# Kernel tuning notes

Measured on AMD Instinct MI355X. Metric: run time of the kernel, lower is better.

## Reference

```python
import jax, jax.numpy as jnp
import numpy as np
from jax.scipy.special import gammainc, gammaln

M, N, D, L, J = 64, 2048, 256, 64, 384  # queries, train points, feat dim, buckets, ncx2 series terms
SIGMA2 = 4.0          # sigma=2.0
BUCKET_SHRINK = 1.0
NEG = -999999.0


def _make_buckets():
    # Mirrors fit(): linspace(ncx2.ppf(1e-4, D*shrink, 0), ncx2.ppf(1-1e-4, D, D*shrink/sigma2)) * sigma2,
    # using the normal approximation to the (non)central chi-square quantiles (scipy unavailable).
    z = 3.7190165  # Phi^{-1}(0.9999)
    df = float(D)
    nc0 = df * BUCKET_SHRINK / SIGMA2
    lb = df * BUCKET_SHRINK - z * np.sqrt(2.0 * df * BUCKET_SHRINK)
    ub = (df + nc0) + z * np.sqrt(2.0 * (df + 2.0 * nc0))
    return jnp.asarray(np.linspace(lb, ub, L) * SIGMA2, dtype=jnp.float32)


def setup_inputs() -> dict:
    key = jax.random.key(0)
    k1, k2, k3 = jax.random.split(key, 3)
    X = jax.random.normal(k1, (M, D), dtype=jnp.float32)
    train_X = jax.random.normal(k2, (N, D), dtype=jnp.float32)
    train_y = jax.random.randint(k3, (N,), 0, 2, dtype=jnp.int32)
    buckets = _make_buckets()
    return {"X": X, "train_X": train_X, "buckets": buckets, "train_y": train_y}


def _ncx2_cdf_matrix(nc, buckets):
    # ncx2.cdf(x, df=D, nc) = sum_j Pois(nc/2)[j] * gammainc(D/2 + j, x/2)
    # nc: [M, N]; buckets are the (already /sigma2) CDF evaluation points x: [L]
    half_nc = nc * 0.5                                            # [M, N]
    j = jnp.arange(J, dtype=jnp.float32)                          # [J]
    logw = (-half_nc[..., None] + j * jnp.log(half_nc)[..., None]
            - gammaln(j + 1.0))                                   # [M, N, J]
    w = jnp.exp(logw)
    G = gammainc(0.5 * D + j[:, None], 0.5 * buckets[None, :])    # [J, L]
    return jnp.einsum('mnj,jl->mnl', w, G)                        # [M, N, L]


def _predict(X, train_X, buckets, train_y):
    # squared euclidean distances, [M, N]
    dists = (jnp.sum(X * X, -1)[:, None] + jnp.sum(train_X * train_X, -1)[None, :]
             - 2.0 * (X @ train_X.T))
    dists = jnp.maximum(dists, 0.0)
    F = _ncx2_cdf_matrix(dists / SIGMA2, buckets / SIGMA2)        # [M, N, L]
    p_mat = jnp.concatenate([F[..., 1:] - F[..., :-1], 1.0 - F[..., -1:]], axis=-1)  # [M, N, L]
    psum = jnp.cumsum(p_mat[..., ::-1], axis=-1)[..., ::-1]       # reverse cumsum over buckets
    logpprod = jnp.cumsum(jnp.log(jnp.maximum(psum, 1e-30)), axis=1)  # scan over train points
    logpprod = jnp.maximum(logpprod, NEG)
    logpprod = jnp.where(jnp.isnan(logpprod), NEG, logpprod)
    # term1[i, l] = logpprod[i-1, l+1] (0 for i==0; NEG at l==L-1 for i>0)
    inner = logpprod[:, :-1, 1:]                                  # [M, N-1, L-1]
    term1 = jnp.concatenate([inner, jnp.full((M, N - 1, 1), NEG, dtype=inner.dtype)], axis=-1)
    term1 = jnp.concatenate([jnp.zeros((M, 1, L), dtype=inner.dtype), term1], axis=1)  # [M, N, L]
    term2 = logpprod[:, -1:, :] - logpprod                        # [M, N, L]
    p = jnp.sum(p_mat * jnp.exp(term1 + term2), axis=-1)          # [M, N] per-point KNN prob
    onehot = jax.nn.one_hot(train_y, 2, dtype=p.dtype)            # [N, 2]
    pred = p @ onehot                                             # [M, 2]
    return pred / jnp.sum(pred, axis=-1, keepdims=True)


def reference(X, train_X, buckets, train_y):
    return _predict(X, train_X, buckets, train_y)
```

## Files before the change

kernel.cpp:

```cpp
#include <hip/hip_runtime.h>
#include <math.h>

#define M_ 64
#define N_ 2048
#define D_ 256
#define L_ 64
#define J_ 384
#define CHUNKS 32
#define CN 64

typedef _Float16 half8 __attribute__((ext_vector_type(8)));
typedef float f32x4 __attribute__((ext_vector_type(4)));

#define OFF_F16   0u
#define OFF_LG8   49152u
#define OFF_INV   49344u
#define OFF_SQX   50880u
#define OFF_PRED  51136u
#define OFF_CHUNK 576000u
#define OFF_PSUM  1657344u

__global__ __launch_bounds__(64)
void k_tab(const float* __restrict__ buckets, const float* __restrict__ Xg,
           char* __restrict__ ws) {
    _Float16* F16 = (_Float16*)(ws + OFF_F16);
    float* lg8  = (float*)(ws + OFF_LG8);
    float* invt = (float*)(ws + OFF_INV);
    float* sqX  = (float*)(ws + OFF_SQX);
    float* pred = (float*)(ws + OFF_PRED);
    int jg = blockIdx.x, l = threadIdx.x;

    if (jg < 12) {
        double x = (double)buckets[l] * 0.125;
        double a = 128.0 + 32.0 * (double)jg;
        double gln = lgamma(a);
        double q;
        if (x < a + 1.0) {
            double ap = a, sum = 1.0 / a, del = sum;
            for (int it = 0; it < 3000; ++it) {
                ap += 1.0; del *= x / ap; sum += del;
                if (fabs(del) < fabs(sum) * 1e-16) break;
            }
            q = 1.0 - sum * exp(-x + a * log(x) - gln);
        } else {
            double b = x + 1.0 - a, c = 1e300, d = 1.0 / b, h = d;
            for (int i = 1; i <= 3000; ++i) {
                double an = -(double)i * ((double)i - a);
                b += 2.0;
                d = an * d + b; if (fabs(d) < 1e-300) d = 1e-300;
                c = b + an / c; if (fabs(c) < 1e-300) c = 1e-300;
                d = 1.0 / d;
                double delc = d * c; h *= delc;
                if (fabs(delc - 1.0) < 1e-16) break;
            }
            q = exp(-x + a * log(x) - gln) * h;
        }
        double tt = exp(a * log(x) - x - lgamma(a + 1.0));
        for (int jj = 0; jj < 32; ++jj) {
            double F = 1.0 - q;
            if (F < 0.0) F = 0.0;
            F16[l * J_ + (jg << 5) + jj] = (_Float16)F;
            q += tt; if (q > 1.0) q = 1.0;
            tt *= x / (a + (double)jj + 1.0);
        }
    } else {
        const float4* xr = (const float4*)(Xg + l * D_);
        float s0 = 0, s1 = 0, s2 = 0, s3 = 0;
        for (int k = 0; k < D_ / 4; ++k) {
            float4 v = xr[k];
            s0 = fmaf(v.x, v.x, s0); s1 = fmaf(v.y, v.y, s1);
            s2 = fmaf(v.z, v.z, s2); s3 = fmaf(v.w, v.w, s3);
        }
        sqX[l] = (s0 + s1) + (s2 + s3);
        if (l < 48) lg8[l] = (float)lgamma(8.0 * (double)l + 1.0);
        for (int i = l; i < J_; i += 64) invt[i] = 1.0f / (float)(i + 1);
        pred[2 * l] = 0.f; pred[2 * l + 1] = 0.f;
    }
}

__global__ __launch_bounds__(128)
void k_fused(const float* __restrict__ Xg, const float* __restrict__ TXg,
             char* __restrict__ ws) {
    const _Float16* F16 = (const _Float16*)(ws + OFF_F16);
    const float* lg8    = (const float*)(ws + OFF_LG8);
    const float* invt   = (const float*)(ws + OFF_INV);
    const float* sqX    = (const float*)(ws + OFF_SQX);
    float* psum         = (float*)(ws + OFF_PSUM);
    double* chunk       = (double*)(ws + OFF_CHUNK);

    __shared__ float  s_dist[64];
    __shared__ double s_part[2][64];

    int bid = blockIdx.x;
    int m = bid >> 5, c = bid & 31;
    int n0 = c << 6;
    int t = threadIdx.x;

    {
        int nloc = t >> 1, half = t & 1;
        const float4* T4 = (const float4*)(TXg + (size_t)(n0 + nloc) * D_ + (half << 7));
        const float4* X4 = (const float4*)(Xg + m * D_ + (half << 7));
        float4 dd{0,0,0,0}, ss{0,0,0,0};
#pragma unroll 8
        for (int k = 0; k < 32; ++k) {
            float4 tv = T4[k], xv = X4[k];
            dd.x = fmaf(xv.x, tv.x, dd.x); dd.y = fmaf(xv.y, tv.y, dd.y);
            dd.z = fmaf(xv.z, tv.z, dd.z); dd.w = fmaf(xv.w, tv.w, dd.w);
            ss.x = fmaf(tv.x, tv.x, ss.x); ss.y = fmaf(tv.y, tv.y, ss.y);
            ss.z = fmaf(tv.z, tv.z, ss.z); ss.w = fmaf(tv.w, tv.w, ss.w);
        }
        float dot = (dd.x + dd.y) + (dd.z + dd.w);
        float st  = (ss.x + ss.y) + (ss.z + ss.w);
        dot += __shfl_xor(dot, 1);
        st  += __shfl_xor(st, 1);
        if (half == 0)
            s_dist[nloc] = fmaxf(sqX[m] + st - 2.f * dot, 0.f);
    }
    __syncthreads();

    int w = t >> 6, l = t & 63;
    int col = l & 15, g = l >> 4;
    int rbase = n0 + (w << 5);

    float la0 = s_dist[(w << 5) + col]      * 0.125f;
    float la1 = s_dist[(w << 5) + 16 + col] * 0.125f;
    float ll0 = __logf(la0), ll1 = __logf(la1);

    f32x4 acc00 = {0,0,0,0}, acc01 = {0,0,0,0}, acc02 = {0,0,0,0}, acc03 = {0,0,0,0};
    f32x4 acc10 = {0,0,0,0}, acc11 = {0,0,0,0}, acc12 = {0,0,0,0}, acc13 = {0,0,0,0};

    for (int s = 0; s < 12; ++s) {
        int jb = (s << 5) + (g << 3);
        float jbf = (float)jb;
        half8 b0 = *(const half8*)(F16 + (size_t)(col     ) * J_ + jb);
        half8 b1 = *(const half8*)(F16 + (size_t)(col + 16) * J_ + jb);
        half8 b2 = *(const half8*)(F16 + (size_t)(col + 32) * J_ + jb);
        half8 b3 = *(const half8*)(F16 + (size_t)(col + 48) * J_ + jb);
        float lgv = lg8[(s << 2) + g];
        float4 iv0 = *(const float4*)(invt + jb);
        float4 iv1 = *(const float4*)(invt + jb + 4);
        {
            float wv = __expf(fmaf(jbf, ll0, -la0 - lgv));
            half8 a;
            a[0] = (_Float16)wv;
            wv *= la0 * iv0.x; a[1] = (_Float16)wv;
            wv *= la0 * iv0.y; a[2] = (_Float16)wv;
            wv *= la0 * iv0.z; a[3] = (_Float16)wv;
            wv *= la0 * iv0.w; a[4] = (_Float16)wv;
            wv *= la0 * iv1.x; a[5] = (_Float16)wv;
            wv *= la0 * iv1.y; a[6] = (_Float16)wv;
            wv *= la0 * iv1.z; a[7] = (_Float16)wv;
            acc00 = __builtin_amdgcn_mfma_f32_16x16x32_f16(a, b0, acc00, 0, 0, 0);
            acc01 = __builtin_amdgcn_mfma_f32_16x16x32_f16(a, b1, acc01, 0, 0, 0);
            acc02 = __builtin_amdgcn_mfma_f32_16x16x32_f16(a, b2, acc02, 0, 0, 0);
            acc03 = __builtin_amdgcn_mfma_f32_16x16x32_f16(a, b3, acc03, 0, 0, 0);
        }
        {
            float wv = __expf(fmaf(jbf, ll1, -la1 - lgv));
            half8 a;
            a[0] = (_Float16)wv;
            wv *= la1 * iv0.x; a[1] = (_Float16)wv;
            wv *= la1 * iv0.y; a[2] = (_Float16)wv;
            wv *= la1 * iv0.z; a[3] = (_Float16)wv;
            wv *= la1 * iv0.w; a[4] = (_Float16)wv;
            wv *= la1 * iv1.x; a[5] = (_Float16)wv;
            wv *= la1 * iv1.y; a[6] = (_Float16)wv;
            wv *= la1 * iv1.z; a[7] = (_Float16)wv;
            acc10 = __builtin_amdgcn_mfma_f32_16x16x32_f16(a, b0, acc10, 0, 0, 0);
            acc11 = __builtin_amdgcn_mfma_f32_16x16x32_f16(a, b1, acc11, 0, 0, 0);
            acc12 = __builtin_amdgcn_mfma_f32_16x16x32_f16(a, b2, acc12, 0, 0, 0);
            acc13 = __builtin_amdgcn_mfma_f32_16x16x32_f16(a, b3, acc13, 0, 0, 0);
        }
    }

    double lsum0 = 0.0, lsum1 = 0.0, lsum2 = 0.0, lsum3 = 0.0;
    float* pbase = psum + (((size_t)(m << 11) + rbase) << 6);
#define EPI(ACC, SP, TI, LS)                                                    \
    {                                                                           \
        _Pragma("unroll")                                                       \
        for (int r = 0; r < 4; ++r) {                                           \
            float ps = 1.f - (ACC)[r];                                          \
            int row = (SP) * 16 + g * 4 + r;                                    \
            pbase[((size_t)row << 6) + (TI) * 16 + col] = ps;                   \
            LS += (double)__logf(fmaxf(ps, 1e-30f));                            \
        }                                                                       \
    }
    EPI(acc00, 0, 0, lsum0) EPI(acc01, 0, 1, lsum1) EPI(acc02, 0, 2, lsum2) EPI(acc03, 0, 3, lsum3)
    EPI(acc10, 1, 0, lsum0) EPI(acc11, 1, 1, lsum1) EPI(acc12, 1, 2, lsum2) EPI(acc13, 1, 3, lsum3)
#undef EPI
    lsum0 += __shfl_xor(lsum0, 16); lsum0 += __shfl_xor(lsum0, 32);
    lsum1 += __shfl_xor(lsum1, 16); lsum1 += __shfl_xor(lsum1, 32);
    lsum2 += __shfl_xor(lsum2, 16); lsum2 += __shfl_xor(lsum2, 32);
    lsum3 += __shfl_xor(lsum3, 16); lsum3 += __shfl_xor(lsum3, 32);
    if (g == 0) {
        s_part[w][col]      = lsum0;
        s_part[w][16 + col] = lsum1;
        s_part[w][32 + col] = lsum2;
        s_part[w][48 + col] = lsum3;
    }
    __syncthreads();
    if (t < 64)
        chunk[((m << 5) + c) * 64 + t] = s_part[0][t] + s_part[1][t];
}

__global__ __launch_bounds__(64)
void k_scan(const int* __restrict__ ty, char* __restrict__ ws) {
    const float* psum   = (const float*)(ws + OFF_PSUM);
    const double* chunk = (const double*)(ws + OFF_CHUNK);
    float* pred         = (float*)(ws + OFF_PRED);
    int b = blockIdx.x, m = b >> 5, c = b & (CHUNKS - 1), l = threadIdx.x;

    double cum = 0.0, T = 0.0;
    for (int c2 = 0; c2 < CHUNKS; ++c2) {
        double v = chunk[((m << 5) + c2) * 64 + l];
        T += v;
        if (c2 < c) cum += v;
    }

    const float* P = psum + (((size_t)m * N_ + (size_t)c * CN) << 6);
    int n0 = c * CN;
    float a0 = 0.f, a1 = 0.f;
    for (int i = 0; i < CN; ++i) {
        float pv = P[((size_t)i << 6) + l];
        float lv = __logf(fmaxf(pv, 1e-30f));
        double nbr = __shfl_down(cum, 1);
        float pvn  = __shfl_down(pv, 1);
        double cin = cum + (double)lv;
        int n = n0 + i;
        double t1 = (n == 0) ? 0.0 : ((l == 63) ? -999999.0 : nbr);
        double t2 = T - cin;
        float e = (float)(t1 + t2);
        float pm = (l == 63) ? pv : (pv - pvn);
        float contrib = pm * __expf(e);
        int y = ty[n];
        a0 += (y == 0) ? contrib : 0.f;
        a1 += (y == 1) ? contrib : 0.f;
        cum = cin;
    }
#pragma unroll
    for (int o = 32; o > 0; o >>= 1) {
        a0 += __shfl_down(a0, o);
        a1 += __shfl_down(a1, o);
    }
    if (l == 0) {
        atomicAdd(&pred[m * 2 + 0], a0);
        atomicAdd(&pred[m * 2 + 1], a1);
    }
}

__global__ __launch_bounds__(64)
void k_norm(char* __restrict__ ws, float* __restrict__ out) {
    const float* pred = (const float*)(ws + OFF_PRED);
    int m = threadIdx.x;
    float a = pred[2 * m], b = pred[2 * m + 1];
    float s = a + b;
    out[2 * m]     = a / s;
    out[2 * m + 1] = b / s;
}

extern "C" void kernel_launch(void* const* d_in, const int* in_sizes, int n_in,
                              void* d_out, int out_size, void* d_ws, size_t ws_size,
                              hipStream_t stream) {
    const float* X       = (const float*)d_in[0];
    const float* train_X = (const float*)d_in[1];
    const float* buckets = (const float*)d_in[2];
    const int*   train_y = (const int*)d_in[3];
    float* out = (float*)d_out;
    char*  ws  = (char*)d_ws;

    k_tab<<<13, 64, 0, stream>>>(buckets, X, ws);
    k_fused<<<M_ * CHUNKS, 128, 0, stream>>>(X, train_X, ws);
    k_scan<<<M_ * CHUNKS, 64, 0, stream>>>(train_y, ws);
    k_norm<<<1, 64, 0, stream>>>(ws, out);
}
```

Measured before the change: 168.1 us.

## Skip negligible Poisson-weight slabs, parallelize gamma table, finer scan chunks

```diff
diff --git a/kernel.cpp b/kernel.cpp
--- a/kernel.cpp
+++ b/kernel.cpp
@@ -4,21 +4,20 @@
 #define M_ 64
 #define N_ 2048
 #define D_ 256
-#define L_ 64
 #define J_ 384
-#define CHUNKS 32
-#define CN 64
+#define C2N 64
+#define CN2 32
 
 typedef _Float16 half8 __attribute__((ext_vector_type(8)));
 typedef float f32x4 __attribute__((ext_vector_type(4)));
 
 #define OFF_F16   0u
 #define OFF_LG8   49152u
-#define OFF_INV   49344u
-#define OFF_SQX   50880u
-#define OFF_PRED  51136u
-#define OFF_CHUNK 576000u
-#define OFF_PSUM  1657344u
+#define OFF_INV   49408u
+#define OFF_SQX   50944u
+#define OFF_PRED  51200u
+#define OFF_CHUNK 51712u
+#define OFF_PSUM  2148864u
 
 __global__ __launch_bounds__(64)
 void k_tab(const float* __restrict__ buckets, const float* __restrict__ Xg,
@@ -30,36 +29,35 @@
     float* pred = (float*)(ws + OFF_PRED);
     int jg = blockIdx.x, l = threadIdx.x;
 
-    if (jg < 12) {
-        double x = (double)buckets[l] * 0.125;
-        double a = 128.0 + 32.0 * (double)jg;
+    if (jg < 48) {
+        const double x = (double)buckets[l] * 0.125;
+        const double a = 128.0 + 8.0 * (double)jg;
         double gln = lgamma(a);
         double q;
         if (x < a + 1.0) {
             double ap = a, sum = 1.0 / a, del = sum;
-            for (int it = 0; it < 3000; ++it) {
+            for (int it = 0; it < 2000; ++it) {
                 ap += 1.0; del *= x / ap; sum += del;
                 if (fabs(del) < fabs(sum) * 1e-16) break;
             }
             q = 1.0 - sum * exp(-x + a * log(x) - gln);
         } else {
-            double b = x + 1.0 - a, c = 1e300, d = 1.0 / b, h = d;
-            for (int i = 1; i <= 3000; ++i) {
+            double b = x + 1.0 - a, cc = 1e300, d = 1.0 / b, h = d;
+            for (int i = 1; i <= 2000; ++i) {
                 double an = -(double)i * ((double)i - a);
                 b += 2.0;
                 d = an * d + b; if (fabs(d) < 1e-300) d = 1e-300;
-                c = b + an / c; if (fabs(c) < 1e-300) c = 1e-300;
+                cc = b + an / cc; if (fabs(cc) < 1e-300) cc = 1e-300;
                 d = 1.0 / d;
-                double delc = d * c; h *= delc;
+                double delc = d * cc; h *= delc;
                 if (fabs(delc - 1.0) < 1e-16) break;
             }
             q = exp(-x + a * log(x) - gln) * h;
         }
         double tt = exp(a * log(x) - x - lgamma(a + 1.0));
-        for (int jj = 0; jj < 32; ++jj) {
-            double F = 1.0 - q;
-            if (F < 0.0) F = 0.0;
-            F16[l * J_ + (jg << 5) + jj] = (_Float16)F;
+        for (int jj = 0; jj < 8; ++jj) {
+            double F = 1.0 - q; if (F < 0.0) F = 0.0;
+            F16[l * J_ + (jg << 3) + jj] = (_Float16)F;
             q += tt; if (q > 1.0) q = 1.0;
             tt *= x / (a + (double)jj + 1.0);
         }
@@ -72,7 +70,7 @@
             s2 = fmaf(v.z, v.z, s2); s3 = fmaf(v.w, v.w, s3);
         }
         sqX[l] = (s0 + s1) + (s2 + s3);
-        if (l < 48) lg8[l] = (float)lgamma(8.0 * (double)l + 1.0);
+        if (l < 49) lg8[l] = (float)lgamma(8.0 * (double)l + 1.0);
         for (int i = l; i < J_; i += 64) invt[i] = 1.0f / (float)(i + 1);
         pred[2 * l] = 0.f; pred[2 * l + 1] = 0.f;
     }
@@ -118,9 +116,9 @@
     }
     __syncthreads();
 
-    int w = t >> 6, l = t & 63;
-    int col = l & 15, g = l >> 4;
-    int rbase = n0 + (w << 5);
+    const int w = t >> 6, l = t & 63;
+    const int col = l & 15, g = l >> 4;
+    const int rbase = n0 + (w << 5);
 
     float la0 = s_dist[(w << 5) + col]      * 0.125f;
     float la1 = s_dist[(w << 5) + 16 + col] * 0.125f;
@@ -130,6 +128,16 @@
     f32x4 acc10 = {0,0,0,0}, acc11 = {0,0,0,0}, acc12 = {0,0,0,0}, acc13 = {0,0,0,0};
 
     for (int s = 0; s < 12; ++s) {
+        float jb0f = (float)(s << 5);
+        float jb1f = jb0f + 32.f;
+        float lgLo = lg8[s << 2], lgHi = lg8[(s << 2) + 4];
+        float e00 = fmaf(jb0f, ll0, -la0) - lgLo;
+        float e01 = fmaf(jb1f, ll0, -la0) - lgHi;
+        float e10 = fmaf(jb0f, ll1, -la1) - lgLo;
+        float e11 = fmaf(jb1f, ll1, -la1) - lgHi;
+        float mx = fmaxf(fmaxf(e00, e01), fmaxf(e10, e11));
+        if (!__any(mx > -35.f)) continue;
+
         int jb = (s << 5) + (g << 3);
         float jbf = (float)jb;
         half8 b0 = *(const half8*)(F16 + (size_t)(col     ) * J_ + jb);
@@ -199,37 +207,43 @@
         s_part[w][48 + col] = lsum3;
     }
     __syncthreads();
-    if (t < 64)
-        chunk[((m << 5) + c) * 64 + t] = s_part[0][t] + s_part[1][t];
-}
-
-__global__ __launch_bounds__(64)
+    {
+        int w2 = t >> 6, l2 = t & 63;
+        chunk[(((m << 6) + (c << 1) + w2) << 6) + l2] = s_part[w2][l2];
+    }
+}
+
+__global__ __launch_bounds__(256)
 void k_scan(const int* __restrict__ ty, char* __restrict__ ws) {
     const float* psum   = (const float*)(ws + OFF_PSUM);
     const double* chunk = (const double*)(ws + OFF_CHUNK);
     float* pred         = (float*)(ws + OFF_PRED);
-    int b = blockIdx.x, m = b >> 5, c = b & (CHUNKS - 1), l = threadIdx.x;
-
+    int b = blockIdx.x;
+    int m = b >> 4, cg = b & 15;
+    int t = threadIdx.x;
+    int w = t >> 6, l = t & 63;
+    int c2 = (cg << 2) + w;
+
+    const double* ch = chunk + ((size_t)(m << 6) << 6) + l;
     double cum = 0.0, T = 0.0;
-    for (int c2 = 0; c2 < CHUNKS; ++c2) {
-        double v = chunk[((m << 5) + c2) * 64 + l];
+    for (int k = 0; k < C2N; ++k) {
+        double v = ch[(size_t)k << 6];
         T += v;
-        if (c2 < c) cum += v;
-    }
-
-    const float* P = psum + (((size_t)m * N_ + (size_t)c * CN) << 6);
-    int n0 = c * CN;
+        if (k < c2) cum += v;
+    }
+
+    const float* P = psum + (((size_t)(m << 11) + (c2 << 5)) << 6);
+    int nb = c2 << 5;
     float a0 = 0.f, a1 = 0.f;
-    for (int i = 0; i < CN; ++i) {
+    for (int i = 0; i < CN2; ++i) {
         float pv = P[((size_t)i << 6) + l];
         float lv = __logf(fmaxf(pv, 1e-30f));
         double nbr = __shfl_down(cum, 1);
         float pvn  = __shfl_down(pv, 1);
         double cin = cum + (double)lv;
-        int n = n0 + i;
+        int n = nb + i;
         double t1 = (n == 0) ? 0.0 : ((l == 63) ? -999999.0 : nbr);
-        double t2 = T - cin;
-        float e = (float)(t1 + t2);
+        float e = (float)(t1 + (T - cin));
         float pm = (l == 63) ? pv : (pv - pvn);
         float contrib = pm * __expf(e);
         int y = ty[n];
@@ -268,8 +282,8 @@
     float* out = (float*)d_out;
     char*  ws  = (char*)d_ws;
 
-    k_tab<<<13, 64, 0, stream>>>(buckets, X, ws);
-    k_fused<<<M_ * CHUNKS, 128, 0, stream>>>(X, train_X, ws);
-    k_scan<<<M_ * CHUNKS, 64, 0, stream>>>(train_y, ws);
+    k_tab<<<49, 64, 0, stream>>>(buckets, X, ws);
+    k_fused<<<M_ * 32, 128, 0, stream>>>(X, train_X, ws);
+    k_scan<<<M_ * 16, 256, 0, stream>>>(train_y, ws);
     k_norm<<<1, 64, 0, stream>>>(ws, out);
 }
```

Result: slower. 179.1 us (+6.6%).
